# Kernel optimization log

Hardware: AMD Instinct MI355X
Metric: run time of the kernel (lower is better)

The kernel has to match this reference:

```python
import jax, jax.numpy as jnp
import numpy as np

N_FEATURES = 512


def _hungarian(cost):
    """Jonker-Volgenant / e-maxx O(n^3) assignment on a square cost matrix.
    Host-side numpy, vectorized inner relaxation. Returns (row_ind, col_ind)
    matching scipy.optimize.linear_sum_assignment for square inputs."""
    n = cost.shape[0]
    INF = np.inf
    u = np.zeros(n + 1)
    v = np.zeros(n + 1)
    p = np.zeros(n + 1, dtype=np.int64)    # p[j] = row matched to column j (1-indexed)
    way = np.zeros(n + 1, dtype=np.int64)
    for i in range(1, n + 1):
        p[0] = i
        j0 = 0
        minv = np.full(n + 1, INF)
        used = np.zeros(n + 1, dtype=bool)
        while True:
            used[j0] = True
            i0 = p[j0]
            free = ~used
            free[0] = False
            cols = np.nonzero(free)[0]
            cur = cost[i0 - 1, cols - 1] - u[i0] - v[cols]
            improve = cur < minv[cols]
            minv[cols] = np.where(improve, cur, minv[cols])
            way[cols] = np.where(improve, j0, way[cols])
            k = int(np.argmin(minv[cols]))
            delta = minv[cols][k]
            j1 = int(cols[k])
            u[p[used]] += delta
            v[used] -= delta
            minv[free] -= delta
            j0 = j1
            if p[j0] == 0:
                break
        while j0:
            j1 = way[j0]
            p[j0] = p[j1]
            j0 = j1
    col_of_row = np.empty(n, dtype=np.int64)
    col_of_row[p[1:] - 1] = np.arange(n)
    return np.arange(n), col_of_row


def setup_inputs() -> dict:
    key = jax.random.key(0)
    k1, k2, k3, k4 = jax.random.split(key, 4)
    n = N_FEATURES
    # Learned diagram parameter, built as in ToFU.__init__ with birth_lims=(0,1), birth_death=True
    b = jax.random.uniform(k1, (n,), dtype=jnp.float32)
    d = b + jax.random.uniform(k2, (n,), dtype=jnp.float32)
    dgm = jnp.stack([b, d], axis=1)            # [n, 2]
    # Target diagram from the data pipeline
    bx = jax.random.uniform(k3, (n,), dtype=jnp.float32)
    dx = bx + jax.random.uniform(k4, (n,), dtype=jnp.float32)
    dgm_x = jnp.stack([bx, dx], axis=1)        # [n, 2]
    return {"dgm": dgm, "dgm_x": dgm_x}


def reference(dgm, dgm_x):
    # --- host-side combinatorial matching (mirrors detach().cpu().numpy() + scipy) ---
    dgm_np = np.asarray(dgm, dtype=np.float64)
    x_np = np.asarray(dgm_x, dtype=np.float64)
    # cdist, euclidean metric: [n, m]
    cost = np.sqrt(((dgm_np[:, None, :] - x_np[None, :, :]) ** 2).sum(-1))
    tofu_idx, target_idx = _hungarian(cost)
    ti = jnp.asarray(tofu_idx)
    ci = jnp.asarray(target_idx)
    # --- differentiable loss (indices are constants; dgm_target rows come from dgm_x) ---
    dgm_target = jax.lax.stop_gradient(dgm).at[ti].set(dgm_x[ci])
    return 0.5 * ((dgm - dgm_target) ** 2).sum()
```

## Files before the change

### kernel.cpp

```cpp
#include <hip/hip_runtime.h>
#include <cfloat>
#include <math.h>

#define N 512
typedef unsigned long long u64_t;

__device__ __forceinline__ u64_t map_f64(double x) {
    u64_t b = (u64_t)__double_as_longlong(x);
    return b ^ ((b >> 63) ? 0xFFFFFFFFFFFFFFFFull : 0x8000000000000000ull);
}
__device__ __forceinline__ double unmap_f64(u64_t b) {
    b ^= ((b >> 63) ? 0x8000000000000000ull : 0xFFFFFFFFFFFFFFFFull);
    return __longlong_as_double((long long)b);
}

__device__ __forceinline__ u64_t wave_min_key(u64_t key) {
    unsigned hi = (unsigned)(key >> 32), lo = (unsigned)key;
#define MIN_STAGE(CTRL)                                                        \
    {                                                                          \
        unsigned oh = (unsigned)__builtin_amdgcn_update_dpp((int)hi, (int)hi,  \
                                                            CTRL, 0xF, 0xF, false); \
        unsigned ol = (unsigned)__builtin_amdgcn_update_dpp((int)lo, (int)lo,  \
                                                            CTRL, 0xF, 0xF, false); \
        const u64_t o = ((u64_t)oh << 32) | ol;                                \
        const u64_t c = ((u64_t)hi << 32) | lo;                                \
        if (o < c) { hi = oh; lo = ol; }                                       \
    }
    MIN_STAGE(0x111) MIN_STAGE(0x112) MIN_STAGE(0x114) MIN_STAGE(0x118)
    MIN_STAGE(0x142) MIN_STAGE(0x143)
#undef MIN_STAGE
    return ((u64_t)hi << 32) | lo;
}

__global__ __launch_bounds__(512, 1) void tofu_solver(
    const float* __restrict__ dgm, const float* __restrict__ dgm_x,
    float* __restrict__ out)
{
#pragma clang fp contract(off)
    __shared__ double2 pt[N];
    __shared__ double  u_lds[N + 1];
    __shared__ int     p_lds[N + 1];
    __shared__ int     way_lds[N + 1];
    __shared__ int     claim[N + 1];
    __shared__ int     flist[4 * N + 32];
    __shared__ u64_t   dslot[3];
    __shared__ u64_t   aslot[2], bslot[2];
    __shared__ double  v1x;
    __shared__ double  red8[8];
    __shared__ int     nfree_s;

    const int tid  = threadIdx.x;
    const int col  = tid + 1;
    const int lane = tid & 63;
    const int wid  = tid >> 6;
    const float2* dgm2  = (const float2*)dgm;
    const float2* dgmx2 = (const float2*)dgm_x;

    {
        const float2 p2 = dgm2[tid];
        pt[tid] = make_double2((double)p2.x, (double)p2.y);
    }
    const float2 q2 = dgmx2[tid];
    const double xb = (double)q2.x, xd = (double)q2.y;
    u_lds[col] = 0.0; p_lds[col] = 0; way_lds[col] = 0; claim[col] = 0x7fffffff;
    if (tid == 0) {
        u_lds[0] = 0.0; p_lds[0] = 0; way_lds[0] = 0; claim[0] = 0x7fffffff;
        dslot[0] = dslot[1] = dslot[2] = ~0ull;
        aslot[0] = aslot[1] = ~0ull; bslot[0] = bslot[1] = ~0ull;
    }
    __syncthreads();

    double v_j; int amin;
    {
        double vsq = DBL_MAX; amin = 1;
        for (int i = 0; i < N; ++i) {
            const double2 rp = pt[i];
            const double db = rp.x - xb, dd = rp.y - xd;
            const double sq = db * db + dd * dd;
            if (sq < vsq) { vsq = sq; amin = i + 1; }
        }
        v_j = sqrt(vsq);
    }

    atomicMin(&claim[amin], col);
    __syncthreads();
    if (claim[amin] == col) p_lds[col] = amin;
    __syncthreads();
    claim[col] = 0;
    __syncthreads();
    { const int r = p_lds[col]; if (r) claim[r] = 1; }
    __syncthreads();
    if (tid == 0) {
        int nf = 0;
        for (int r = 1; r <= N; ++r) if (!claim[r]) flist[nf++] = r;
        nfree_s = nf;
    }
    __syncthreads();

    {
        int head = 0, tail = nfree_s, q = 0;
        const int cap = 3 * tail + 16;
        int myp = p_lds[col];
        for (int step = 0; step < cap && head < tail; ++step) {
            const int i = flist[head++];
            const double2 rp = pt[i - 1];
            const double db = rp.x - xb, dd = rp.y - xd;
            const double val = sqrt(db * db + dd * dd) - v_j;
            const u64_t key = (map_f64(val) & ~0x7FFFFull)
                            | ((u64_t)(col - 1) << 10) | (u64_t)myp;
            u64_t kr = wave_min_key(key);
            if (lane == 63) atomicMin(&aslot[q], kr);
            __syncthreads();
            const u64_t k1 = aslot[q];
            const int j1    = (int)((k1 >> 10) & 511) + 1;
            const int k_old = (int)(k1 & 1023);
            if (col == j1) v1x = val;
            kr = wave_min_key((col == j1) ? ~0ull : key);
            if (lane == 63) atomicMin(&bslot[q], kr);
            __syncthreads();
            const double m2t = unmap_f64(bslot[q] & ~0x7FFFFull);
            const double v1e = v1x;
            const double ui  = fmax(m2t, v1e);
            if (col == j1) { v_j -= (ui - val); myp = i; }
            if (tid == 0) {
                u_lds[i] = ui;
                p_lds[j1] = i;
                if (k_old) flist[tail] = k_old;
                aslot[q ^ 1] = ~0ull; bslot[q ^ 1] = ~0ull;
            }
            if (k_old) ++tail;
            q ^= 1;
            __syncthreads();
        }
    }

    claim[col] = 0;
    __syncthreads();
    { const int r = p_lds[col]; if (r) claim[r] = 1; }
    __syncthreads();
    if (tid == 0) {
        int nf = 0;
        for (int r = 1; r <= N; ++r) if (!claim[r]) flist[nf++] = r;
        nfree_s = nf;
    }
    __syncthreads();
    const int nfree = nfree_s;

    for (int kk = 0; kk < nfree; ++kk) {
        const int iroot = flist[kk];
        const int pcol  = p_lds[col];
        if (tid == 0) p_lds[0] = iroot;
        double minv = DBL_MAX, du = 0.0, du0 = 0.0;
        bool used = false;
        int juse = 0, i0 = iroot, par = 0;

        while (true) {
            if (col == juse) used = true;
            const double2 rp = pt[i0 - 1];
            const double u0 = u_lds[i0];
            u64_t key = ~0ull;
            if (!used) {
                const double db = rp.x - xb, dd = rp.y - xd;
                const double c = sqrt(db * db + dd * dd);
                const double cur = (c - u0) - v_j;
                if (cur < minv) { minv = cur; way_lds[col] = juse; }
                key = (map_f64(minv) & ~0x7FFFFull)
                    | ((u64_t)(col - 1) << 10) | (u64_t)pcol;
            }
            key = wave_min_key(key);
            if (lane == 63) atomicMin(&dslot[par], key);
            __syncthreads();
            const u64_t k = dslot[par];
            if (tid == 0) dslot[(par + 2) % 3] = ~0ull;
            const double delta = unmap_f64(k & ~0x7FFFFull);
            if (used) { v_j -= delta; du += delta; }
            else        minv -= delta;
            if (tid == 0) du0 += delta;
            juse = (int)((k >> 10) & 511) + 1;
            i0   = (int)(k & 1023);
            if (i0 == 0) break;
            par = (par + 1) % 3;
        }

        if (used) u_lds[pcol] += du;
        if (tid == 0) {
            u_lds[iroot] += du0;
            dslot[par] = ~0ull;
            int j = juse;
            while (j) { const int jn = way_lds[j]; p_lds[j] = p_lds[jn]; j = jn; }
        }
        __syncthreads();
    }

    const int r = p_lds[col] - 1;
    const float2 a = dgm2[r];
    const float2 b = dgmx2[tid];
    const float fb = a.x - b.x;
    const float fd = a.y - b.y;
    double acc = (double)fb * (double)fb + (double)fd * (double)fd;
    #pragma unroll
    for (int m = 32; m >= 1; m >>= 1) acc += __shfl_xor(acc, m, 64);
    if (lane == 0) red8[wid] = acc;
    __syncthreads();
    if (tid == 0) {
        double s = 0.0;
        #pragma unroll
        for (int w = 0; w < 8; ++w) s += red8[w];
        out[0] = (float)(0.5 * s);
    }
}

extern "C" void kernel_launch(void* const* d_in, const int* in_sizes, int n_in,
                              void* d_out, int out_size, void* d_ws, size_t ws_size,
                              hipStream_t stream) {
    const float* dgm   = (const float*)d_in[0];
    const float* dgm_x = (const float*)d_in[1];
    float* out = (float*)d_out;
    tofu_solver<<<1, 512, 0, stream>>>(dgm, dgm_x, out);
}
```

Before: 5.754 ms.

## Add row-side reduction-transfer rounds before augmenting-row-reduction in LAPJV solver

Adds three rounds of a row-wise reduction/transfer pass after column reduction. In each round every row computes its minimum reduced cost over all columns. Matched rows update their dual u and their matched column's v. Unmatched rows claim a free argmin column through an atomic. The goal is to leave fewer free rows for the serial augmenting-row-reduction and the Dijkstra-style augmentation, which cost one barrier per step. In exchange each round adds an O(N) distance scan per thread, extra LDS arrays, and new dual updates that must keep the reduced costs consistent.

```diff
diff --git a/kernel.cpp b/kernel.cpp
--- a/kernel.cpp
+++ b/kernel.cpp
@@ -3,6 +3,7 @@
 #include <math.h>
 
 #define N 512
+#define TG_ROUNDS 3
 typedef unsigned long long u64_t;
 
 __device__ __forceinline__ u64_t map_f64(double x) {
@@ -38,9 +39,12 @@
 {
 #pragma clang fp contract(off)
     __shared__ double2 pt[N];
+    __shared__ double2 ptx[N];
+    __shared__ double  v_arr[N + 1];
     __shared__ double  u_lds[N + 1];
     __shared__ int     p_lds[N + 1];
     __shared__ int     way_lds[N + 1];
+    __shared__ int     mcol[N + 1];
     __shared__ int     claim[N + 1];
     __shared__ int     flist[4 * N + 32];
     __shared__ u64_t   dslot[3];
@@ -59,12 +63,15 @@
     {
         const float2 p2 = dgm2[tid];
         pt[tid] = make_double2((double)p2.x, (double)p2.y);
-    }
-    const float2 q2 = dgmx2[tid];
-    const double xb = (double)q2.x, xd = (double)q2.y;
-    u_lds[col] = 0.0; p_lds[col] = 0; way_lds[col] = 0; claim[col] = 0x7fffffff;
-    if (tid == 0) {
-        u_lds[0] = 0.0; p_lds[0] = 0; way_lds[0] = 0; claim[0] = 0x7fffffff;
+        const float2 q2 = dgmx2[tid];
+        ptx[tid] = make_double2((double)q2.x, (double)q2.y);
+    }
+    const double xb = ptx[tid].x, xd = ptx[tid].y;
+    u_lds[col] = 0.0; p_lds[col] = 0; way_lds[col] = 0;
+    mcol[col] = 0; claim[col] = 0x7fffffff;
+    if (tid == 0) {
+        u_lds[0] = 0.0; p_lds[0] = 0; way_lds[0] = 0; mcol[0] = 0;
+        claim[0] = 0x7fffffff;
         dslot[0] = dslot[1] = dslot[2] = ~0ull;
         aslot[0] = aslot[1] = ~0ull; bslot[0] = bslot[1] = ~0ull;
     }
@@ -86,6 +93,41 @@
     __syncthreads();
     if (claim[amin] == col) p_lds[col] = amin;
     __syncthreads();
+    if (p_lds[col] != 0) mcol[p_lds[col]] = col;
+    v_arr[col] = v_j;
+    __syncthreads();
+
+    const double2 rp_own = pt[tid];
+    for (int round = 0; round < TG_ROUNDS; ++round) {
+        claim[col] = 0x7fffffff;
+        const int row = col;
+        const int mc  = mcol[row];
+        double mu1 = DBL_MAX; int jmin = 1;
+        for (int j = 0; j < N; ++j) {
+            const double2 xp = ptx[j];
+            const double vv = v_arr[j + 1];
+            const double db = rp_own.x - xp.x, dd = rp_own.y - xp.y;
+            const double cv = sqrt(db * db + dd * dd) - vv;
+            if (mc) { if (j + 1 != mc && cv < mu1) mu1 = cv; }
+            else    { if (cv < mu1) { mu1 = cv; jmin = j + 1; } }
+        }
+        __syncthreads();
+        if (mc) {
+            const double2 xp = ptx[mc - 1];
+            const double db = rp_own.x - xp.x, dd = rp_own.y - xp.y;
+            u_lds[row] = mu1;
+            v_arr[mc] = sqrt(db * db + dd * dd) - mu1;
+        } else if (p_lds[jmin] == 0) {
+            atomicMin(&claim[jmin], row);
+        }
+        __syncthreads();
+        if (!mc && claim[jmin] == row) {
+            p_lds[jmin] = row; mcol[row] = jmin; u_lds[row] = mu1;
+        }
+        __syncthreads();
+    }
+    v_j = v_arr[col];
+
     claim[col] = 0;
     __syncthreads();
     { const int r = p_lds[col]; if (r) claim[r] = 1; }
@@ -119,8 +161,7 @@
             if (lane == 63) atomicMin(&bslot[q], kr);
             __syncthreads();
             const double m2t = unmap_f64(bslot[q] & ~0x7FFFFull);
-            const double v1e = v1x;
-            const double ui  = fmax(m2t, v1e);
+            const double ui  = fmax(m2t, v1x);
             if (col == j1) { v_j -= (ui - val); myp = i; }
             if (tid == 0) {
                 u_lds[i] = ui;
```

Measured after the change: 6.459 ms. +12.2%, slower.

## Halve block to 256 threads with two columns per thread and packed row data

Applied to the files above, without the earlier changes.

The solver now runs with 256 threads, each owning two columns. Each thread takes the min over its own two columns before the wave reduction, so cross-wave atomic reductions and barriers involve four waves instead of eight. Row points are packed as float bits together with the dual u into one double2 in LDS, so each step needs a single LDS load. The cost is twice the per-thread arithmetic (sqrt and compares) on the serial critical path, plus possible wave_min_key behaviour changes with fewer waves.

```diff
diff --git a/kernel.cpp b/kernel.cpp
--- a/kernel.cpp
+++ b/kernel.cpp
@@ -3,6 +3,7 @@
 #include <math.h>
 
 #define N 512
+#define T 256
 typedef unsigned long long u64_t;
 
 __device__ __forceinline__ u64_t map_f64(double x) {
@@ -32,13 +33,20 @@
     return ((u64_t)hi << 32) | lo;
 }
 
-__global__ __launch_bounds__(512, 1) void tofu_solver(
+__device__ __forceinline__ void rd_decode(const double2 rd, double& b, double& d,
+                                          double& u) {
+    const u64_t bits = (u64_t)__double_as_longlong(rd.x);
+    b = (double)__uint_as_float((unsigned)bits);
+    d = (double)__uint_as_float((unsigned)(bits >> 32));
+    u = rd.y;
+}
+
+__global__ __launch_bounds__(T, 1) void tofu_solver(
     const float* __restrict__ dgm, const float* __restrict__ dgm_x,
     float* __restrict__ out)
 {
 #pragma clang fp contract(off)
-    __shared__ double2 pt[N];
-    __shared__ double  u_lds[N + 1];
+    __shared__ double2 rowdat[N + 1];
     __shared__ int     p_lds[N + 1];
     __shared__ int     way_lds[N + 1];
     __shared__ int     claim[N + 1];
@@ -46,49 +54,69 @@
     __shared__ u64_t   dslot[3];
     __shared__ u64_t   aslot[2], bslot[2];
     __shared__ double  v1x;
-    __shared__ double  red8[8];
+    __shared__ double  red4[4];
     __shared__ int     nfree_s;
 
     const int tid  = threadIdx.x;
-    const int col  = tid + 1;
     const int lane = tid & 63;
     const int wid  = tid >> 6;
+    const int colv[2] = { tid + 1, tid + 1 + T };
     const float2* dgm2  = (const float2*)dgm;
     const float2* dgmx2 = (const float2*)dgm_x;
 
-    {
-        const float2 p2 = dgm2[tid];
-        pt[tid] = make_double2((double)p2.x, (double)p2.y);
-    }
-    const float2 q2 = dgmx2[tid];
-    const double xb = (double)q2.x, xd = (double)q2.y;
-    u_lds[col] = 0.0; p_lds[col] = 0; way_lds[col] = 0; claim[col] = 0x7fffffff;
-    if (tid == 0) {
-        u_lds[0] = 0.0; p_lds[0] = 0; way_lds[0] = 0; claim[0] = 0x7fffffff;
+    #pragma unroll
+    for (int c = 0; c < 2; ++c) {
+        const int r = colv[c];
+        const float2 p2 = dgm2[r - 1];
+        double2 rd;
+        rd.x = __longlong_as_double((long long)(
+                   ((u64_t)__float_as_uint(p2.y) << 32) | __float_as_uint(p2.x)));
+        rd.y = 0.0;
+        rowdat[r] = rd;
+        p_lds[r] = 0; way_lds[r] = 0; claim[r] = 0x7fffffff;
+    }
+    double xb[2], xd[2];
+    #pragma unroll
+    for (int c = 0; c < 2; ++c) {
+        const float2 q2 = dgmx2[colv[c] - 1];
+        xb[c] = (double)q2.x; xd[c] = (double)q2.y;
+    }
+    if (tid == 0) {
+        p_lds[0] = 0; way_lds[0] = 0; claim[0] = 0x7fffffff;
         dslot[0] = dslot[1] = dslot[2] = ~0ull;
         aslot[0] = aslot[1] = ~0ull; bslot[0] = bslot[1] = ~0ull;
     }
     __syncthreads();
 
-    double v_j; int amin;
+    double v[2]; int amin[2];
     {
-        double vsq = DBL_MAX; amin = 1;
-        for (int i = 0; i < N; ++i) {
-            const double2 rp = pt[i];
-            const double db = rp.x - xb, dd = rp.y - xd;
-            const double sq = db * db + dd * dd;
-            if (sq < vsq) { vsq = sq; amin = i + 1; }
-        }
-        v_j = sqrt(vsq);
-    }
-
-    atomicMin(&claim[amin], col);
-    __syncthreads();
-    if (claim[amin] == col) p_lds[col] = amin;
-    __syncthreads();
-    claim[col] = 0;
-    __syncthreads();
-    { const int r = p_lds[col]; if (r) claim[r] = 1; }
+        double vsq[2] = { DBL_MAX, DBL_MAX };
+        amin[0] = amin[1] = 1;
+        for (int i = 1; i <= N; ++i) {
+            const double2 rd = rowdat[i];
+            double rb, rdd, ru; rd_decode(rd, rb, rdd, ru);
+            #pragma unroll
+            for (int c = 0; c < 2; ++c) {
+                const double db = rb - xb[c], dd = rdd - xd[c];
+                const double sq = db * db + dd * dd;
+                if (sq < vsq[c]) { vsq[c] = sq; amin[c] = i; }
+            }
+        }
+        v[0] = sqrt(vsq[0]); v[1] = sqrt(vsq[1]);
+    }
+
+    int myp[2] = { 0, 0 };
+    #pragma unroll
+    for (int c = 0; c < 2; ++c) atomicMin(&claim[amin[c]], colv[c]);
+    __syncthreads();
+    #pragma unroll
+    for (int c = 0; c < 2; ++c)
+        if (claim[amin[c]] == colv[c]) { p_lds[colv[c]] = amin[c]; myp[c] = amin[c]; }
+    __syncthreads();
+
+    for (int c = 0; c < 2; ++c) claim[colv[c]] = 0;
+    __syncthreads();
+    for (int c = 0; c < 2; ++c) { const int r = p_lds[colv[c]]; if (r) claim[r] = 1; }
     __syncthreads();
     if (tid == 0) {
         int nf = 0;
@@ -100,30 +128,40 @@
     {
         int head = 0, tail = nfree_s, q = 0;
         const int cap = 3 * tail + 16;
-        int myp = p_lds[col];
         for (int step = 0; step < cap && head < tail; ++step) {
             const int i = flist[head++];
-            const double2 rp = pt[i - 1];
-            const double db = rp.x - xb, dd = rp.y - xd;
-            const double val = sqrt(db * db + dd * dd) - v_j;
-            const u64_t key = (map_f64(val) & ~0x7FFFFull)
-                            | ((u64_t)(col - 1) << 10) | (u64_t)myp;
-            u64_t kr = wave_min_key(key);
+            const double2 rd = rowdat[i];
+            double rb, rdd, ru; rd_decode(rd, rb, rdd, ru);
+            double val[2]; u64_t key[2];
+            #pragma unroll
+            for (int c = 0; c < 2; ++c) {
+                const double db = rb - xb[c], dd = rdd - xd[c];
+                val[c] = sqrt(db * db + dd * dd) - v[c];
+                key[c] = (map_f64(val[c]) & ~0x7FFFFull)
+                       | ((u64_t)(colv[c] - 1) << 10) | (u64_t)myp[c];
+            }
+            u64_t kr = wave_min_key(key[0] < key[1] ? key[0] : key[1]);
             if (lane == 63) atomicMin(&aslot[q], kr);
             __syncthreads();
             const u64_t k1 = aslot[q];
             const int j1    = (int)((k1 >> 10) & 511) + 1;
             const int k_old = (int)(k1 & 1023);
-            if (col == j1) v1x = val;
-            kr = wave_min_key((col == j1) ? ~0ull : key);
+            u64_t kmin2 = ~0ull;
+            #pragma unroll
+            for (int c = 0; c < 2; ++c) {
+                if (colv[c] == j1) v1x = val[c];
+                else if (key[c] < kmin2) kmin2 = key[c];
+            }
+            kr = wave_min_key(kmin2);
             if (lane == 63) atomicMin(&bslot[q], kr);
             __syncthreads();
             const double m2t = unmap_f64(bslot[q] & ~0x7FFFFull);
-            const double v1e = v1x;
-            const double ui  = fmax(m2t, v1e);
-            if (col == j1) { v_j -= (ui - val); myp = i; }
+            const double ui  = fmax(m2t, v1x);
+            #pragma unroll
+            for (int c = 0; c < 2; ++c)
+                if (colv[c] == j1) { v[c] -= (ui - val[c]); myp[c] = i; }
             if (tid == 0) {
-                u_lds[i] = ui;
+                rowdat[i].y = ui;
                 p_lds[j1] = i;
                 if (k_old) flist[tail] = k_old;
                 aslot[q ^ 1] = ~0ull; bslot[q ^ 1] = ~0ull;
@@ -134,9 +172,9 @@
         }
     }
 
-    claim[col] = 0;
-    __syncthreads();
-    { const int r = p_lds[col]; if (r) claim[r] = 1; }
+    for (int c = 0; c < 2; ++c) claim[colv[c]] = 0;
+    __syncthreads();
+    for (int c = 0; c < 2; ++c) { const int r = p_lds[colv[c]]; if (r) claim[r] = 1; }
     __syncthreads();
     if (tid == 0) {
         int nf = 0;
@@ -148,33 +186,40 @@
 
     for (int kk = 0; kk < nfree; ++kk) {
         const int iroot = flist[kk];
-        const int pcol  = p_lds[col];
+        const int pc[2] = { p_lds[colv[0]], p_lds[colv[1]] };
         if (tid == 0) p_lds[0] = iroot;
-        double minv = DBL_MAX, du = 0.0, du0 = 0.0;
-        bool used = false;
-        int juse = 0, i0 = iroot, par = 0;
+        double minv[2] = { DBL_MAX, DBL_MAX }, du[2] = { 0.0, 0.0 }, du0 = 0.0;
+        int usedm = 0, juse = 0, i0 = iroot, par = 0;
 
         while (true) {
-            if (col == juse) used = true;
-            const double2 rp = pt[i0 - 1];
-            const double u0 = u_lds[i0];
-            u64_t key = ~0ull;
-            if (!used) {
-                const double db = rp.x - xb, dd = rp.y - xd;
-                const double c = sqrt(db * db + dd * dd);
-                const double cur = (c - u0) - v_j;
-                if (cur < minv) { minv = cur; way_lds[col] = juse; }
-                key = (map_f64(minv) & ~0x7FFFFull)
-                    | ((u64_t)(col - 1) << 10) | (u64_t)pcol;
-            }
-            key = wave_min_key(key);
-            if (lane == 63) atomicMin(&dslot[par], key);
+            if (colv[0] == juse) usedm |= 1;
+            if (colv[1] == juse) usedm |= 2;
+            const double2 rd = rowdat[i0];
+            double rb, rdd, u0; rd_decode(rd, rb, rdd, u0);
+            u64_t kmin = ~0ull;
+            #pragma unroll
+            for (int c = 0; c < 2; ++c) {
+                if (!((usedm >> c) & 1)) {
+                    const double db = rb - xb[c], dd = rdd - xd[c];
+                    const double cost = sqrt(db * db + dd * dd);
+                    const double cur = (cost - u0) - v[c];
+                    if (cur < minv[c]) { minv[c] = cur; way_lds[colv[c]] = juse; }
+                    const u64_t k = (map_f64(minv[c]) & ~0x7FFFFull)
+                                  | ((u64_t)(colv[c] - 1) << 10) | (u64_t)pc[c];
+                    if (k < kmin) kmin = k;
+                }
+            }
+            kmin = wave_min_key(kmin);
+            if (lane == 63) atomicMin(&dslot[par], kmin);
             __syncthreads();
             const u64_t k = dslot[par];
             if (tid == 0) dslot[(par + 2) % 3] = ~0ull;
             const double delta = unmap_f64(k & ~0x7FFFFull);
-            if (used) { v_j -= delta; du += delta; }
-            else        minv -= delta;
+            #pragma unroll
+            for (int c = 0; c < 2; ++c) {
+                if ((usedm >> c) & 1) { v[c] -= delta; du[c] += delta; }
+                else                    minv[c] -= delta;
+            }
             if (tid == 0) du0 += delta;
             juse = (int)((k >> 10) & 511) + 1;
             i0   = (int)(k & 1023);
@@ -182,9 +227,10 @@
             par = (par + 1) % 3;
         }
 
-        if (used) u_lds[pcol] += du;
+        if (usedm & 1) rowdat[pc[0]].y += du[0];
+        if (usedm & 2) rowdat[pc[1]].y += du[1];
         if (tid == 0) {
-            u_lds[iroot] += du0;
+            rowdat[iroot].y += du0;
             dslot[par] = ~0ull;
             int j = juse;
             while (j) { const int jn = way_lds[j]; p_lds[j] = p_lds[jn]; j = jn; }
@@ -192,20 +238,25 @@
         __syncthreads();
     }
 
-    const int r = p_lds[col] - 1;
-    const float2 a = dgm2[r];
-    const float2 b = dgmx2[tid];
-    const float fb = a.x - b.x;
-    const float fd = a.y - b.y;
-    double acc = (double)fb * (double)fb + (double)fd * (double)fd;
+    double acc = 0.0;
+    #pragma unroll
+    for (int c = 0; c < 2; ++c) {
+        const int j = colv[c] - 1;
+        const int r = p_lds[colv[c]] - 1;
+        const float2 a = dgm2[r];
+        const float2 b = dgmx2[j];
+        const float fb = a.x - b.x;
+        const float fd = a.y - b.y;
+        acc += (double)fb * (double)fb + (double)fd * (double)fd;
+    }
     #pragma unroll
     for (int m = 32; m >= 1; m >>= 1) acc += __shfl_xor(acc, m, 64);
-    if (lane == 0) red8[wid] = acc;
+    if (lane == 0) red4[wid] = acc;
     __syncthreads();
     if (tid == 0) {
         double s = 0.0;
         #pragma unroll
-        for (int w = 0; w < 8; ++w) s += red8[w];
+        for (int w = 0; w < 4; ++w) s += red4[w];
         out[0] = (float)(0.5 * s);
     }
 }
@@ -216,5 +267,5 @@
     const float* dgm   = (const float*)d_in[0];
     const float* dgm_x = (const float*)d_in[1];
     float* out = (float*)d_out;
-    tofu_solver<<<1, 512, 0, stream>>>(dgm, dgm_x, out);
-}
+    tofu_solver<<<1, T, 0, stream>>>(dgm, dgm_x, out);
+}
```

Result: slower. 6.719 ms (+16.8%).

## Pack row data with duals and tighten free-column potentials before augmentations

Applied to the files above, without the earlier changes.

Packs each row's float birth/death coordinates and its dual u into a single double2 LDS entry, so one LDS load serves the inner relaxation. Before each augmentation it raises the v potential of unmatched columns to the minimum reduced cost over all rows, updated incrementally from a change list of rows whose u moved. This tightening is meant to shorten the Dijkstra-style searches. In exchange it adds a full N-row scan up front, per-augmentation rescans of changed rows, and an extra barrier.

```diff
diff --git a/kernel.cpp b/kernel.cpp
--- a/kernel.cpp
+++ b/kernel.cpp
@@ -32,22 +32,30 @@
     return ((u64_t)hi << 32) | lo;
 }
 
+__device__ __forceinline__ void rd_decode(const double2 rd, double& b, double& d,
+                                          double& u) {
+    const u64_t bits = (u64_t)__double_as_longlong(rd.x);
+    b = (double)__uint_as_float((unsigned)bits);
+    d = (double)__uint_as_float((unsigned)(bits >> 32));
+    u = rd.y;
+}
+
 __global__ __launch_bounds__(512, 1) void tofu_solver(
     const float* __restrict__ dgm, const float* __restrict__ dgm_x,
     float* __restrict__ out)
 {
 #pragma clang fp contract(off)
-    __shared__ double2 pt[N];
-    __shared__ double  u_lds[N + 1];
+    __shared__ double2 rowdat[N + 1];
     __shared__ int     p_lds[N + 1];
     __shared__ int     way_lds[N + 1];
     __shared__ int     claim[N + 1];
     __shared__ int     flist[4 * N + 32];
+    __shared__ int     chg[N + 8];
     __shared__ u64_t   dslot[3];
     __shared__ u64_t   aslot[2], bslot[2];
     __shared__ double  v1x;
     __shared__ double  red8[8];
-    __shared__ int     nfree_s;
+    __shared__ int     nfree_s, nchg;
 
     const int tid  = threadIdx.x;
     const int col  = tid + 1;
@@ -58,34 +66,43 @@
 
     {
         const float2 p2 = dgm2[tid];
-        pt[tid] = make_double2((double)p2.x, (double)p2.y);
+        double2 rd;
+        rd.x = __longlong_as_double((long long)(
+                   ((u64_t)__float_as_uint(p2.y) << 32) | __float_as_uint(p2.x)));
+        rd.y = 0.0;
+        rowdat[col] = rd;
     }
     const float2 q2 = dgmx2[tid];
     const double xb = (double)q2.x, xd = (double)q2.y;
-    u_lds[col] = 0.0; p_lds[col] = 0; way_lds[col] = 0; claim[col] = 0x7fffffff;
-    if (tid == 0) {
-        u_lds[0] = 0.0; p_lds[0] = 0; way_lds[0] = 0; claim[0] = 0x7fffffff;
+    p_lds[col] = 0; way_lds[col] = 0; claim[col] = 0x7fffffff;
+    if (tid == 0) {
+        rowdat[0] = make_double2(0.0, 0.0);
+        p_lds[0] = 0; way_lds[0] = 0; claim[0] = 0x7fffffff;
         dslot[0] = dslot[1] = dslot[2] = ~0ull;
         aslot[0] = aslot[1] = ~0ull; bslot[0] = bslot[1] = ~0ull;
+        nchg = 0;
     }
     __syncthreads();
 
     double v_j; int amin;
     {
         double vsq = DBL_MAX; amin = 1;
-        for (int i = 0; i < N; ++i) {
-            const double2 rp = pt[i];
-            const double db = rp.x - xb, dd = rp.y - xd;
+        for (int i = 1; i <= N; ++i) {
+            const double2 rd = rowdat[i];
+            double rb, rdd, ru; rd_decode(rd, rb, rdd, ru);
+            const double db = rb - xb, dd = rdd - xd;
             const double sq = db * db + dd * dd;
-            if (sq < vsq) { vsq = sq; amin = i + 1; }
+            if (sq < vsq) { vsq = sq; amin = i; }
         }
         v_j = sqrt(vsq);
     }
 
+    int myp = 0;
     atomicMin(&claim[amin], col);
     __syncthreads();
-    if (claim[amin] == col) p_lds[col] = amin;
-    __syncthreads();
+    if (claim[amin] == col) { p_lds[col] = amin; myp = amin; }
+    __syncthreads();
+
     claim[col] = 0;
     __syncthreads();
     { const int r = p_lds[col]; if (r) claim[r] = 1; }
@@ -100,11 +117,11 @@
     {
         int head = 0, tail = nfree_s, q = 0;
         const int cap = 3 * tail + 16;
-        int myp = p_lds[col];
         for (int step = 0; step < cap && head < tail; ++step) {
             const int i = flist[head++];
-            const double2 rp = pt[i - 1];
-            const double db = rp.x - xb, dd = rp.y - xd;
+            const double2 rd = rowdat[i];
+            double rb, rdd, ru; rd_decode(rd, rb, rdd, ru);
+            const double db = rb - xb, dd = rdd - xd;
             const double val = sqrt(db * db + dd * dd) - v_j;
             const u64_t key = (map_f64(val) & ~0x7FFFFull)
                             | ((u64_t)(col - 1) << 10) | (u64_t)myp;
@@ -119,11 +136,10 @@
             if (lane == 63) atomicMin(&bslot[q], kr);
             __syncthreads();
             const double m2t = unmap_f64(bslot[q] & ~0x7FFFFull);
-            const double v1e = v1x;
-            const double ui  = fmax(m2t, v1e);
+            const double ui  = fmax(m2t, v1x);
             if (col == j1) { v_j -= (ui - val); myp = i; }
             if (tid == 0) {
-                u_lds[i] = ui;
+                rowdat[i].y = ui;
                 p_lds[j1] = i;
                 if (k_old) flist[tail] = k_old;
                 aslot[q ^ 1] = ~0ull; bslot[q ^ 1] = ~0ull;
@@ -146,21 +162,40 @@
     __syncthreads();
     const int nfree = nfree_s;
 
+    double mtight = DBL_MAX;
+    for (int i = 1; i <= N; ++i) {
+        const double2 rd = rowdat[i];
+        double rb, rdd, ru; rd_decode(rd, rb, rdd, ru);
+        const double db = rb - xb, dd = rdd - xd;
+        mtight = fmin(mtight, sqrt(db * db + dd * dd) - ru);
+    }
+    if (p_lds[col] == 0) v_j = fmax(v_j, mtight);
+
     for (int kk = 0; kk < nfree; ++kk) {
         const int iroot = flist[kk];
-        const int pcol  = p_lds[col];
-        if (tid == 0) p_lds[0] = iroot;
+        const int nc = nchg;
+        for (int k = 0; k < nc; ++k) {
+            const int r = chg[k];
+            const double2 rd = rowdat[r];
+            double rb, rdd, ru; rd_decode(rd, rb, rdd, ru);
+            const double db = rb - xb, dd = rdd - xd;
+            mtight = fmin(mtight, sqrt(db * db + dd * dd) - ru);
+        }
+        if (p_lds[col] == 0) v_j = fmax(v_j, mtight);
+        __syncthreads();
+        if (tid == 0) { nchg = 0; p_lds[0] = iroot; }
+        const int pcol = p_lds[col];
         double minv = DBL_MAX, du = 0.0, du0 = 0.0;
         bool used = false;
         int juse = 0, i0 = iroot, par = 0;
 
         while (true) {
             if (col == juse) used = true;
-            const double2 rp = pt[i0 - 1];
-            const double u0 = u_lds[i0];
+            const double2 rd = rowdat[i0];
+            double rb, rdd, u0; rd_decode(rd, rb, rdd, u0);
             u64_t key = ~0ull;
             if (!used) {
-                const double db = rp.x - xb, dd = rp.y - xd;
+                const double db = rb - xb, dd = rdd - xd;
                 const double c = sqrt(db * db + dd * dd);
                 const double cur = (c - u0) - v_j;
                 if (cur < minv) { minv = cur; way_lds[col] = juse; }
@@ -182,9 +217,15 @@
             par = (par + 1) % 3;
         }
 
-        if (used) u_lds[pcol] += du;
+        if (used) {
+            rowdat[pcol].y += du;
+            const int ix = atomicAdd(&nchg, 1);
+            chg[ix] = pcol;
+        }
         if (tid == 0) {
-            u_lds[iroot] += du0;
+            rowdat[iroot].y += du0;
+            const int ix = atomicAdd(&nchg, 1);
+            chg[ix] = iroot;
             dslot[par] = ~0ull;
             int j = juse;
             while (j) { const int jn = way_lds[j]; p_lds[j] = p_lds[jn]; j = jn; }
```

Result: slower. 7.210 ms (+25.3%).
